# Performance work log

Hardware: AMD Instinct MI355X
Metric: run time of the kernel (lower is better)

## Reference

```python
import jax, jax.numpy as jnp
import numpy as np

EPS = 1e-6
K_MEM, C_MEM = 512, 2048
SEQ, BATCH = 256, 16
NUM_LAYERS, NUM_HEADS, HEAD_DIM = 12, 12, 64
KV_DIM = NUM_LAYERS * NUM_HEADS * HEAD_DIM * 2  # 18432
NOISE_STD = 0.01
PINV_STEPS = 3
BEN_COHEN_INIT = -5.0


def approx_pinv(A, steps=PINV_STEPS):
    # Ben-Cohen iterative pseudoinverse. A: (B, M, N) -> (B, N, M)
    alpha = jnp.minimum(jnp.exp(jnp.float32(BEN_COHEN_INIT)), jnp.float32(5e-4))  # clamp(max=5e-4)
    P = alpha * jnp.swapaxes(A, -2, -1)
    for _ in range(steps):
        P = 2.0 * P - (P @ A) @ P  # matches bmm(bmm(P, A), P)
    return P


def setup_inputs() -> dict:
    key = jax.random.key(0)
    ks = jax.random.split(key, 6)
    lim = np.sqrt(6.0 / (C_MEM + KV_DIM))  # xavier_uniform
    return {
        "z_sequence": jax.random.normal(ks[0], (SEQ, BATCH, C_MEM), jnp.float32),
        "z_query": jax.random.normal(ks[1], (BATCH, C_MEM), jnp.float32),
        "noise": jax.random.normal(ks[2], (SEQ, BATCH, C_MEM), jnp.float32),
        "memory_mean": jax.random.normal(ks[3], (K_MEM, C_MEM), jnp.float32) * 0.02,
        "memory_logvar": jnp.zeros((K_MEM,), jnp.float32),
        "w_logvar": jnp.zeros((1,), jnp.float32),
        "W_M_weight": jax.random.uniform(ks[4], (KV_DIM, C_MEM), jnp.float32, -lim, lim),
    }


def reference(z_sequence, z_query, noise, memory_mean, memory_logvar, w_logvar, W_M_weight):
    B = z_query.shape[0]
    # ---- write ----
    prior_var = jnp.exp(memory_logvar) + EPS                     # (K,)
    prior_mean_b = jnp.broadcast_to(memory_mean, (B, K_MEM, C_MEM))
    z_noise = z_sequence + noise * NOISE_STD                     # (S, B, C)
    z_t = jnp.swapaxes(z_noise, 0, 1)                            # (B, S, C)
    M_pinv = approx_pinv(prior_mean_b)                           # (B, C, K)
    w = z_t @ M_pinv                                             # (B, S, K)
    w_pinv = approx_pinv(w)                                      # (B, K, S)
    new_memory_mean = w_pinv @ z_t                               # (B, K, C)
    # KL divergence (post_var == prior_var here)
    t1 = C_MEM * jnp.sum(prior_var / prior_var)
    t2 = jnp.sum((new_memory_mean - prior_mean_b) ** 2 / prior_var[None, :, None], axis=(-2, -1))
    t3 = -jnp.float32(C_MEM * K_MEM)
    t4 = C_MEM * jnp.sum(jnp.log(prior_var) - jnp.log(prior_var))
    dkl_M = jnp.mean(t1 + t2 + t3 + t4)
    # ---- read (deterministic addressing) ----
    M_pinv2 = approx_pinv(new_memory_mean)                       # (B, C, K)
    w_mean = jnp.einsum('bc,bck->bk', z_query, M_pinv2)          # (B, K)
    z_retrieved = jnp.einsum('bk,bkc->bc', w_mean, new_memory_mean)  # (B, C)
    Z_r_kv = z_retrieved @ W_M_weight.T                          # (B, kv_dim)
    wl = jnp.broadcast_to(w_logvar, w_mean.shape)
    dkl_w = 0.5 * jnp.sum(jnp.exp(wl) + w_mean ** 2 - 1.0 - wl)
    return z_retrieved, Z_r_kv, dkl_M, dkl_w
```

## Files before the change

### kernel.cpp

```cpp
#include <hip/hip_runtime.h>

#define ALPHA 5.0e-4f

typedef short s16x8 __attribute__((ext_vector_type(8)));
typedef unsigned short u16x8 __attribute__((ext_vector_type(8)));
typedef float f32x4 __attribute__((ext_vector_type(4)));

__device__ __forceinline__ unsigned short f2bf(float f) {
    unsigned int u = __builtin_bit_cast(unsigned int, f);
    u += 0x7fffu + ((u >> 16) & 1u);
    return (unsigned short)(u >> 16);
}
__device__ __forceinline__ float bf2f(unsigned short h) {
    return __builtin_bit_cast(float, (unsigned int)h << 16);
}
__device__ __forceinline__ f32x4 mfma16(s16x8 a, s16x8 b, f32x4 c) {
    return __builtin_amdgcn_mfma_f32_16x16x32_bf16(a, b, c, 0, 0, 0);
}

template<int ROWS>
__device__ __forceinline__ void stage_kcontig(const float* __restrict__ src, int ld,
                                              unsigned short* __restrict__ lds, int tid)
{
#pragma unroll
    for (int it = 0; it < ROWS * 8 / 256; ++it) {
        const int g = tid + it * 256;
        const int row = g >> 3, s = g & 7;
        const float* p = src + (long long)row * ld + s * 8;
        const float4 x0 = *(const float4*)p;
        const float4 x1 = *(const float4*)(p + 4);
        u16x8 h;
        h[0] = f2bf(x0.x); h[1] = f2bf(x0.y); h[2] = f2bf(x0.z); h[3] = f2bf(x0.w);
        h[4] = f2bf(x1.x); h[5] = f2bf(x1.y); h[6] = f2bf(x1.z); h[7] = f2bf(x1.w);
        *(u16x8*)(lds + row * 64 + ((s ^ (row & 7)) << 3)) = h;
    }
}

template<int ROWS>
__device__ __forceinline__ void stage_kstrided(const float* __restrict__ src, int ld,
                                               unsigned short* __restrict__ lds, int tid)
{
    constexpr int KPT = ROWS * 64 / 256;
    const int m = tid % ROWS, kb = (tid / ROWS) * KPT;
#pragma unroll
    for (int j8 = 0; j8 < KPT / 8; ++j8) {
        u16x8 h;
#pragma unroll
        for (int j = 0; j < 8; ++j)
            h[j] = f2bf(src[(long long)(kb + j8 * 8 + j) * ld + m]);
        const int s = (kb >> 3) + j8;
        *(u16x8*)(lds + m * 64 + ((s ^ (m & 7)) << 3)) = h;
    }
}

template<int ROWS>
__device__ __forceinline__ void stage_kcontig_b(const unsigned short* __restrict__ src, int ld,
                                                unsigned short* __restrict__ lds, int tid)
{
#pragma unroll
    for (int it = 0; it < ROWS * 8 / 256; ++it) {
        const int g = tid + it * 256;
        const int row = g >> 3, s = g & 7;
        const u16x8 h = *(const u16x8*)(src + (long long)row * ld + s * 8);
        *(u16x8*)(lds + row * 64 + ((s ^ (row & 7)) << 3)) = h;
    }
}

template<int ROWS>
__device__ __forceinline__ void stage_kstrided_b(const unsigned short* __restrict__ src, int ld,
                                                 unsigned short* __restrict__ lds, int tid)
{
    constexpr int KPT = ROWS * 64 / 256;
    const int m = tid % ROWS, kb = (tid / ROWS) * KPT;
#pragma unroll
    for (int j8 = 0; j8 < KPT / 8; ++j8) {
        u16x8 h;
#pragma unroll
        for (int j = 0; j < 8; ++j)
            h[j] = src[(long long)(kb + j8 * 8 + j) * ld + m];
        const int s = (kb >> 3) + j8;
        *(u16x8*)(lds + m * 64 + ((s ^ (m & 7)) << 3)) = h;
    }
}

template<int BM, int BN, bool TA, bool TB, bool ABF, bool BBF, bool OBF,
         bool OT, bool CINT, bool ATOM = false>
__device__ __forceinline__
void gemm_dev(int bx, int by, int bz,
              const void* __restrict__ Av, int lda, long long sA,
              const void* __restrict__ Bv, int ldb, long long sB,
              void* __restrict__ Dv, int ldd, long long sD,
              const float* __restrict__ Cin, long long sC,
              float alpha, float beta, int Kd)
{
    constexpr int TWM = BM / 2, TWN = BN / 2;
    constexpr int FM = TWM / 16, FN = TWN / 16;
    __shared__ unsigned short As[BM * 64];
    __shared__ unsigned short Bs[BN * 64];

    const int tid = threadIdx.x;
    const int lane = tid & 63, w = tid >> 6;
    const int wm = w >> 1, wn = w & 1;
    const int lrow = lane & 15, lk = lane >> 4;
    const int m0 = by * BM, n0 = bx * BN;

    f32x4 acc[FM][FN];
#pragma unroll
    for (int i = 0; i < FM; ++i)
#pragma unroll
        for (int j = 0; j < FN; ++j) acc[i][j] = (f32x4){0.f, 0.f, 0.f, 0.f};

    for (int k0 = 0; k0 < Kd; k0 += 64) {
        if (ABF) {
            const unsigned short* Ab = (const unsigned short*)Av + (long long)bz * sA;
            if (!TA) stage_kcontig_b<BM>(Ab + (long long)m0 * lda + k0, lda, As, tid);
            else     stage_kstrided_b<BM>(Ab + (long long)k0 * lda + m0, lda, As, tid);
        } else {
            const float* Ab = (const float*)Av + (long long)bz * sA;
            if (!TA) stage_kcontig<BM>(Ab + (long long)m0 * lda + k0, lda, As, tid);
            else     stage_kstrided<BM>(Ab + (long long)k0 * lda + m0, lda, As, tid);
        }
        if (BBF) {
            const unsigned short* Bb = (const unsigned short*)Bv + (long long)bz * sB;
            if (TB)  stage_kcontig_b<BN>(Bb + (long long)n0 * ldb + k0, ldb, Bs, tid);
            else     stage_kstrided_b<BN>(Bb + (long long)k0 * ldb + n0, ldb, Bs, tid);
        } else {
            const float* Bb = (const float*)Bv + (long long)bz * sB;
            if (TB)  stage_kcontig<BN>(Bb + (long long)n0 * ldb + k0, ldb, Bs, tid);
            else     stage_kstrided<BN>(Bb + (long long)k0 * ldb + n0, ldb, Bs, tid);
        }
        __syncthreads();
#pragma unroll
        for (int kk = 0; kk < 2; ++kk) {
            s16x8 ah[FM], bh[FN];
#pragma unroll
            for (int i = 0; i < FM; ++i) {
                const int row = wm * TWM + i * 16 + lrow;
                const int s = kk * 4 + lk;
                ah[i] = *(const s16x8*)(As + row * 64 + ((s ^ (row & 7)) << 3));
            }
#pragma unroll
            for (int j = 0; j < FN; ++j) {
                const int col = wn * TWN + j * 16 + lrow;
                const int s = kk * 4 + lk;
                bh[j] = *(const s16x8*)(Bs + col * 64 + ((s ^ (col & 7)) << 3));
            }
#pragma unroll
            for (int i = 0; i < FM; ++i)
#pragma unroll
                for (int j = 0; j < FN; ++j)
                    acc[i][j] = mfma16(ah[i], bh[j], acc[i][j]);
        }
        __syncthreads();
    }

#pragma unroll
    for (int i = 0; i < FM; ++i)
#pragma unroll
        for (int j = 0; j < FN; ++j) {
            const int col = n0 + wn * TWN + j * 16 + lrow;
#pragma unroll
            for (int r = 0; r < 4; ++r) {
                const int row = m0 + wm * TWM + i * 16 + lk * 4 + r;
                float v = alpha * acc[i][j][r];
                if (Cin) {
                    const float cv = CINT ? Cin[(long long)col * sC + row]
                                          : Cin[(long long)row * ldd + col];
                    v = fmaf(beta, cv, v);
                }
                if (ATOM) {
                    atomicAdd((float*)Dv + (long long)row * ldd + col, v);
                } else if (OT) {
                    ((unsigned short*)Dv)[(long long)(row >> 8) * sD +
                                          (long long)col * ldd + (row & 255)] = f2bf(v);
                } else if (OBF) {
                    ((unsigned short*)Dv + (long long)bz * sD)[(long long)row * ldd + col] = f2bf(v);
                } else {
                    ((float*)Dv + (long long)bz * sD)[(long long)row * ldd + col] = v;
                }
            }
        }
}

template<int BM, int BN, bool TA, bool TB, bool ABF, bool BBF, bool OBF,
         bool OT = false, bool CINT = false>
__global__ __launch_bounds__(256)
void gemm_mfma(const void* __restrict__ Av, int lda, long long sA,
               const void* __restrict__ Bv, int ldb, long long sB,
               void* __restrict__ Dv, int ldd, long long sD,
               const float* __restrict__ Cin, long long sC,
               float alpha, float beta, int Kd)
{
    gemm_dev<BM, BN, TA, TB, ABF, BBF, OBF, OT, CINT>(
        blockIdx.x, blockIdx.y, blockIdx.z,
        Av, lda, sA, Bv, ldb, sB, Dv, ldd, sD, Cin, sC, alpha, beta, Kd);
}

__global__ __launch_bounds__(256)
void fused_prep_kernel(const float* __restrict__ zs, const float* __restrict__ no,
                       const float* __restrict__ zq, const float* __restrict__ mm,
                       unsigned short* __restrict__ ztb, float* __restrict__ q,
                       float* __restrict__ G1)
{
    const int blk = blockIdx.x, t = threadIdx.x;
    if (blk < 4096) {
        const int bs = blk;
        const int b = bs >> 8, sI = bs & 255;
        const long long in = ((long long)sI * 16 + b) * 2048 + t * 8;
        const f32x4 z0 = __builtin_nontemporal_load((const f32x4*)(zs + in));
        const f32x4 z1 = __builtin_nontemporal_load((const f32x4*)(zs + in + 4));
        const f32x4 n0 = __builtin_nontemporal_load((const f32x4*)(no + in));
        const f32x4 n1 = __builtin_nontemporal_load((const f32x4*)(no + in + 4));
        float zf[8];
#pragma unroll
        for (int j = 0; j < 4; ++j) {
            zf[j]     = fmaf(0.01f, n0[j], z0[j]);
            zf[j + 4] = fmaf(0.01f, n1[j], z1[j]);
        }
        u16x8 o;
#pragma unroll
        for (int j = 0; j < 8; ++j) o[j] = f2bf(zf[j]);
        *(u16x8*)(ztb + ((long long)bs * 2048 + t * 8)) = o;
        const float4 q0 = *(const float4*)(zq + b * 2048 + t * 8);
        const float4 q1 = *(const float4*)(zq + b * 2048 + t * 8 + 4);
        float qa = zf[0] * q0.x + zf[1] * q0.y + zf[2] * q0.z + zf[3] * q0.w
                 + zf[4] * q1.x + zf[5] * q1.y + zf[6] * q1.z + zf[7] * q1.w;
        __shared__ float red[256];
        red[t] = qa; __syncthreads();
        for (int st = 128; st > 0; st >>= 1) { if (t < st) red[t] += red[t + st]; __syncthreads(); }
        if (t == 0) q[bs] = red[0];
    } else {
        const int g = blk - 4096;
        const int ky = g & 7;
        const int tile = g >> 3;
        gemm_dev<64, 64, false, true, false, false, false, false, false, true>(
            tile & 7, tile >> 3, 0,
            mm + ky * 256, 2048, 0, mm + ky * 256, 2048, 0,
            G1, 512, 0, nullptr, 0, 1.f, 0.f, 256);
    }
}

__global__ __launch_bounds__(256)
void wT_u_kernel(const unsigned short* __restrict__ ztb,
                 const unsigned short* __restrict__ P1b,
                 unsigned short* __restrict__ wTb,
                 const float* __restrict__ q, float* __restrict__ wmean)
{
    constexpr int BM = 128, BN = 64, TWM = 64, TWN = 32, FM = 4, FN = 2;
    __shared__ unsigned short As[BM * 64];
    __shared__ unsigned short Bs[BN * 64];
    const int lin = blockIdx.x;
    const int r = lin & 7, tt = lin >> 3;
    const int by = r + 8 * (tt & 3), bx = tt >> 2;
    const int tid = threadIdx.x;
    const int lane = tid & 63, w = tid >> 6;
    const int wm = w >> 1, wn = w & 1;
    const int lrow = lane & 15, lk = lane >> 4;
    const int m0 = by * BM, n0 = bx * BN;

    f32x4 acc[FM][FN];
#pragma unroll
    for (int i = 0; i < FM; ++i)
#pragma unroll
        for (int j = 0; j < FN; ++j) acc[i][j] = (f32x4){0.f, 0.f, 0.f, 0.f};

    for (int k0 = 0; k0 < 2048; k0 += 64) {
        stage_kcontig_b<BM>(ztb + (long long)m0 * 2048 + k0, 2048, As, tid);
        stage_kstrided_b<BN>(P1b + (long long)k0 * 512 + n0, 512, Bs, tid);
        __syncthreads();
#pragma unroll
        for (int kk = 0; kk < 2; ++kk) {
            s16x8 ah[FM], bh[FN];
#pragma unroll
            for (int i = 0; i < FM; ++i) {
                const int row = wm * TWM + i * 16 + lrow;
                const int s = kk * 4 + lk;
                ah[i] = *(const s16x8*)(As + row * 64 + ((s ^ (row & 7)) << 3));
            }
#pragma unroll
            for (int j = 0; j < FN; ++j) {
                const int col = wn * TWN + j * 16 + lrow;
                const int s = kk * 4 + lk;
                bh[j] = *(const s16x8*)(Bs + col * 64 + ((s ^ (col & 7)) << 3));
            }
#pragma unroll
            for (int i = 0; i < FM; ++i)
#pragma unroll
                for (int j = 0; j < FN; ++j)
                    acc[i][j] = mfma16(ah[i], bh[j], acc[i][j]);
        }
        __syncthreads();
    }

    float up[FN] = {0.f, 0.f};
#pragma unroll
    for (int i = 0; i < FM; ++i)
#pragma unroll
        for (int rr = 0; rr < 4; ++rr) {
            const int row = m0 + wm * TWM + i * 16 + lk * 4 + rr;
            const float qv = q[row];
#pragma unroll
            for (int j = 0; j < FN; ++j) {
                const int col = n0 + wn * TWN + j * 16 + lrow;
                const float v = acc[i][j][rr];
                wTb[(long long)(row >> 8) * 131072 + (long long)col * 256 + (row & 255)] = f2bf(v);
                up[j] = fmaf(v, qv, up[j]);
            }
        }
    const int b = m0 >> 8;
#pragma unroll
    for (int j = 0; j < FN; ++j) {
        float v = up[j];
        v += __shfl_xor(v, 16);
        v += __shfl_xor(v, 32);
        if (lk == 0) {
            const int col = n0 + wn * TWN + j * 16 + lrow;
            atomicAdd(&wmean[b * 512 + col], (64.0f * ALPHA * ALPHA) * v);
        }
    }
}

__global__ __launch_bounds__(256)
void tail1_kernel(const unsigned short* __restrict__ wTb,
                  const unsigned short* __restrict__ ztb,
                  const float* __restrict__ wmean, const float* __restrict__ wlv,
                  float* __restrict__ out)
{
    __shared__ __align__(16) float smemf[1024];
    const int blk = blockIdx.x, tid = threadIdx.x;
    if (blk < 256) {
        float* wms = smemf;
        float* ys  = smemf + 512;
        float* red2 = smemf + 768;
        const int r8 = blk & 7, t8 = blk >> 3;
        const int b = r8 + 8 * (t8 & 1), ct = t8 >> 1;
        wms[tid] = wmean[b * 512 + tid];
        wms[tid + 256] = wmean[b * 512 + 256 + tid];
        __syncthreads();
        {
            const unsigned short* wp = wTb + (long long)b * 131072 + tid;
            float yv = 0.f;
#pragma unroll 8
            for (int k = 0; k < 512; ++k)
                yv = fmaf(wms[k], bf2f(wp[(long long)k * 256]), yv);
            ys[tid] = yv;
        }
        __syncthreads();
        const int c = ct * 128 + (tid & 127), sh = tid >> 7;
        const unsigned short* zp = ztb + (long long)b * 524288 + c;
        float acc2 = 0.f;
        const int sbase = sh * 128;
#pragma unroll 8
        for (int s = 0; s < 128; ++s)
            acc2 = fmaf(ys[sbase + s], bf2f(zp[(long long)(sbase + s) * 2048]), acc2);
        red2[tid] = acc2; __syncthreads();
        if (sh == 0)
            out[(long long)b * 2048 + c] = (8.0f * ALPHA) * (red2[tid] + red2[tid + 128]);
    } else {
        float* red = smemf;
        float s = 0.f;
        for (int i = tid; i < 16 * 512; i += 256) { const float v = wmean[i]; s += v * v; }
        red[tid] = s; __syncthreads();
        for (int st = 128; st > 0; st >>= 1) { if (tid < st) red[tid] += red[tid + st]; __syncthreads(); }
        if (tid == 0) {
            const float l = wlv[0];
            out[327681] = 0.5f * (red[0] + 8192.0f * (expf(l) - 1.0f - l));
        }
    }
}

__global__ __launch_bounds__(256)
void tail2_kernel(const unsigned short* __restrict__ wTb,
                  const unsigned short* __restrict__ ztb,
                  const float* __restrict__ mm, const float* __restrict__ mlv,
                  const float* __restrict__ WM, float* __restrict__ out)
{
    __shared__ __align__(16) unsigned char smem[34304];
    const int g = blockIdx.x, tid = threadIdx.x;
    const int grp = g / 26, p = g % 26;
    if (p < 8) {
        constexpr int BM = 128, BN = 128, TWM = 64, TWN = 64, FM = 4, FN = 4;
        unsigned short* As = (unsigned short*)smem;
        unsigned short* Bs = As + BM * 64;
        float* ivars = (float*)(smem + 32768);
        float* red = (float*)(smem + 33280);
        const int bz = ((2 * grp + p) & 7) + 8 * (grp & 1);
        const int rest = grp >> 1;
        const int by = rest & 3, bx = rest >> 2;
        const int lane = tid & 63, w = tid >> 6;
        const int wm = w >> 1, wn = w & 1;
        const int lrow = lane & 15, lk = lane >> 4;
        const int m0 = by * BM, n0 = bx * BN;

        if (tid < 128) ivars[tid] = 1.0f / (expf(mlv[m0 + tid]) + 1e-6f);

        f32x4 acc[FM][FN];
#pragma unroll
        for (int i = 0; i < FM; ++i)
#pragma unroll
            for (int j = 0; j < FN; ++j) acc[i][j] = (f32x4){0.f, 0.f, 0.f, 0.f};

        for (int k0 = 0; k0 < 256; k0 += 64) {
            stage_kcontig_b<BM>(wTb + (long long)bz * 131072 + (long long)m0 * 256 + k0, 256, As, tid);
            stage_kstrided_b<BN>(ztb + (long long)bz * 524288 + (long long)k0 * 2048 + n0, 2048, Bs, tid);
            __syncthreads();
#pragma unroll
            for (int kk = 0; kk < 2; ++kk) {
                s16x8 ah[FM], bh[FN];
#pragma unroll
                for (int i = 0; i < FM; ++i) {
                    const int row = wm * TWM + i * 16 + lrow;
                    const int s = kk * 4 + lk;
                    ah[i] = *(const s16x8*)(As + row * 64 + ((s ^ (row & 7)) << 3));
                }
#pragma unroll
                for (int j = 0; j < FN; ++j) {
                    const int col = wn * TWN + j * 16 + lrow;
                    const int s = kk * 4 + lk;
                    bh[j] = *(const s16x8*)(Bs + col * 64 + ((s ^ (col & 7)) << 3));
                }
#pragma unroll
                for (int i = 0; i < FM; ++i)
#pragma unroll
                    for (int j = 0; j < FN; ++j)
                        acc[i][j] = mfma16(ah[i], bh[j], acc[i][j]);
            }
            __syncthreads();
        }

        const float A8 = 8.0f * ALPHA;
        float da = 0.f;
#pragma unroll
        for (int i = 0; i < FM; ++i)
#pragma unroll
            for (int j = 0; j < FN; ++j) {
                const int cl = wn * TWN + j * 16 + lrow;
#pragma unroll
                for (int rr = 0; rr < 4; ++rr) {
                    const int rl = wm * TWM + i * 16 + lk * 4 + rr;
                    const float v = A8 * acc[i][j][rr];
                    const float d = v - mm[(long long)(m0 + rl) * 2048 + (n0 + cl)];
                    da = fmaf(d * d, ivars[rl], da);
                }
            }
        red[tid] = da; __syncthreads();
        for (int st = 128; st > 0; st >>= 1) { if (tid < st) red[tid] += red[tid + st]; __syncthreads(); }
        if (tid == 0) atomicAdd(&out[327680], red[0] * (1.0f / 16.0f));
    } else {
        const int z = grp * 18 + (p - 8);
        const int bx = z % 288, ky = z / 288;
        const int lane = tid & 63, w = tid >> 6;
        const int d0 = bx * 64 + w * 16;
        const int kc0 = ky * 256;
        const int rr = lane & 15, kq = lane >> 4;
        const float* zr = out;
        s16x8 areg[8];
        const float* zb = zr + rr * 2048 + kc0 + kq * 8;
#pragma unroll
        for (int s = 0; s < 8; ++s) {
            const f32x4 a0 = *(const f32x4*)(zb + s * 32);
            const f32x4 a1 = *(const f32x4*)(zb + s * 32 + 4);
            u16x8 h;
#pragma unroll
            for (int j = 0; j < 4; ++j) { h[j] = f2bf(a0[j]); h[j + 4] = f2bf(a1[j]); }
            areg[s] = __builtin_bit_cast(s16x8, h);
        }
        f32x4 acc = {0.f, 0.f, 0.f, 0.f};
        const float* wb = WM + (long long)(d0 + rr) * 2048 + kc0 + kq * 8;
#pragma unroll
        for (int s = 0; s < 8; ++s) {
            const f32x4 b0 = __builtin_nontemporal_load((const f32x4*)(wb + s * 32));
            const f32x4 b1 = __builtin_nontemporal_load((const f32x4*)(wb + s * 32 + 4));
            u16x8 h;
#pragma unroll
            for (int j = 0; j < 4; ++j) { h[j] = f2bf(b0[j]); h[j + 4] = f2bf(b1[j]); }
            acc = mfma16(areg[s], __builtin_bit_cast(s16x8, h), acc);
        }
        float* oz = out + 32768;
#pragma unroll
        for (int r = 0; r < 4; ++r)
            atomicAdd(&oz[(long long)(kq * 4 + r) * 18432 + d0 + rr], acc[r]);
    }
}

extern "C" void kernel_launch(void* const* d_in, const int* in_sizes, int n_in,
                              void* d_out, int out_size, void* d_ws, size_t ws_size,
                              hipStream_t stream)
{
    (void)in_sizes; (void)n_in; (void)out_size; (void)ws_size;
    const float* z_seq   = (const float*)d_in[0];
    const float* z_query = (const float*)d_in[1];
    const float* noise   = (const float*)d_in[2];
    const float* mm      = (const float*)d_in[3];
    const float* mlv     = (const float*)d_in[4];
    const float* wlv     = (const float*)d_in[5];
    const float* WM      = (const float*)d_in[6];
    float* out = (float*)d_out;

    char* wsb = (char*)d_ws;
    unsigned short* ztb  = (unsigned short*)(wsb);
    unsigned short* wTb  = (unsigned short*)(wsb + (16LL << 20));
    float*          G1   = (float*)(wsb + (24LL << 20));
    float*          wmean = (float*)(wsb + (25LL << 20));
    unsigned short* P1b  = (unsigned short*)(wsb + (26LL << 20));
    float*          qvec = (float*)(wsb + (30LL << 20));

    hipMemsetAsync(G1, 0, (1u << 20) + 32768, stream);
    hipMemsetAsync(out + 32768, 0, (294912 + 1) * sizeof(float), stream);
    fused_prep_kernel<<<4608, 256, 0, stream>>>(z_seq, noise, z_query, mm,
                                                ztb, qvec, G1);
    gemm_mfma<64,64,true,false,false,false,true,false,true><<<dim3(8,32,1),256,0,stream>>>(
        mm,2048,0, G1,512,0, P1b,512,0, mm,2048,
        -28.0f*ALPHA*ALPHA, 8.0f*ALPHA, 512);
    wT_u_kernel<<<256,256,0,stream>>>(ztb, P1b, wTb, qvec, wmean);
    tail1_kernel<<<257,256,0,stream>>>(wTb, ztb, wmean, wlv, out);
    tail2_kernel<<<3328,256,0,stream>>>(wTb, ztb, mm, mlv, WM, out);
}
```

Before: 177.6 us.

## Replace atomic split-K Gram with partial buffers, fold memsets into P1 kernel

```diff
diff --git a/kernel.cpp b/kernel.cpp
--- a/kernel.cpp
+++ b/kernel.cpp
@@ -83,15 +83,12 @@
     }
 }
 
-template<int BM, int BN, bool TA, bool TB, bool ABF, bool BBF, bool OBF,
-         bool OT, bool CINT, bool ATOM = false>
+template<int BM, int BN, bool TA, bool TB>
 __device__ __forceinline__
-void gemm_dev(int bx, int by, int bz,
-              const void* __restrict__ Av, int lda, long long sA,
-              const void* __restrict__ Bv, int ldb, long long sB,
-              void* __restrict__ Dv, int ldd, long long sD,
-              const float* __restrict__ Cin, long long sC,
-              float alpha, float beta, int Kd)
+void gemm_dev_f32(int bx, int by,
+                  const float* __restrict__ A, int lda,
+                  const float* __restrict__ B, int ldb,
+                  float* __restrict__ D, int ldd, int Kd)
 {
     constexpr int TWM = BM / 2, TWN = BN / 2;
     constexpr int FM = TWM / 16, FN = TWN / 16;
@@ -111,24 +108,10 @@
         for (int j = 0; j < FN; ++j) acc[i][j] = (f32x4){0.f, 0.f, 0.f, 0.f};
 
     for (int k0 = 0; k0 < Kd; k0 += 64) {
-        if (ABF) {
-            const unsigned short* Ab = (const unsigned short*)Av + (long long)bz * sA;
-            if (!TA) stage_kcontig_b<BM>(Ab + (long long)m0 * lda + k0, lda, As, tid);
-            else     stage_kstrided_b<BM>(Ab + (long long)k0 * lda + m0, lda, As, tid);
-        } else {
-            const float* Ab = (const float*)Av + (long long)bz * sA;
-            if (!TA) stage_kcontig<BM>(Ab + (long long)m0 * lda + k0, lda, As, tid);
-            else     stage_kstrided<BM>(Ab + (long long)k0 * lda + m0, lda, As, tid);
-        }
-        if (BBF) {
-            const unsigned short* Bb = (const unsigned short*)Bv + (long long)bz * sB;
-            if (TB)  stage_kcontig_b<BN>(Bb + (long long)n0 * ldb + k0, ldb, Bs, tid);
-            else     stage_kstrided_b<BN>(Bb + (long long)k0 * ldb + n0, ldb, Bs, tid);
-        } else {
-            const float* Bb = (const float*)Bv + (long long)bz * sB;
-            if (TB)  stage_kcontig<BN>(Bb + (long long)n0 * ldb + k0, ldb, Bs, tid);
-            else     stage_kstrided<BN>(Bb + (long long)k0 * ldb + n0, ldb, Bs, tid);
-        }
+        if (!TA) stage_kcontig<BM>(A + (long long)m0 * lda + k0, lda, As, tid);
+        else     stage_kstrided<BM>(A + (long long)k0 * lda + m0, lda, As, tid);
+        if (TB)  stage_kcontig<BN>(B + (long long)n0 * ldb + k0, ldb, Bs, tid);
+        else     stage_kstrided<BN>(B + (long long)k0 * ldb + n0, ldb, Bs, tid);
         __syncthreads();
 #pragma unroll
         for (int kk = 0; kk < 2; ++kk) {
@@ -162,49 +145,28 @@
 #pragma unroll
             for (int r = 0; r < 4; ++r) {
                 const int row = m0 + wm * TWM + i * 16 + lk * 4 + r;
-                float v = alpha * acc[i][j][r];
-                if (Cin) {
-                    const float cv = CINT ? Cin[(long long)col * sC + row]
-                                          : Cin[(long long)row * ldd + col];
-                    v = fmaf(beta, cv, v);
-                }
-                if (ATOM) {
-                    atomicAdd((float*)Dv + (long long)row * ldd + col, v);
-                } else if (OT) {
-                    ((unsigned short*)Dv)[(long long)(row >> 8) * sD +
-                                          (long long)col * ldd + (row & 255)] = f2bf(v);
-                } else if (OBF) {
-                    ((unsigned short*)Dv + (long long)bz * sD)[(long long)row * ldd + col] = f2bf(v);
-                } else {
-                    ((float*)Dv + (long long)bz * sD)[(long long)row * ldd + col] = v;
-                }
-            }
-        }
-}
-
-template<int BM, int BN, bool TA, bool TB, bool ABF, bool BBF, bool OBF,
-         bool OT = false, bool CINT = false>
-__global__ __launch_bounds__(256)
-void gemm_mfma(const void* __restrict__ Av, int lda, long long sA,
-               const void* __restrict__ Bv, int ldb, long long sB,
-               void* __restrict__ Dv, int ldd, long long sD,
-               const float* __restrict__ Cin, long long sC,
-               float alpha, float beta, int Kd)
-{
-    gemm_dev<BM, BN, TA, TB, ABF, BBF, OBF, OT, CINT>(
-        blockIdx.x, blockIdx.y, blockIdx.z,
-        Av, lda, sA, Bv, ldb, sB, Dv, ldd, sD, Cin, sC, alpha, beta, Kd);
+                D[(long long)row * ldd + col] = acc[i][j][r];
+            }
+        }
 }
 
 __global__ __launch_bounds__(256)
 void fused_prep_kernel(const float* __restrict__ zs, const float* __restrict__ no,
                        const float* __restrict__ zq, const float* __restrict__ mm,
                        unsigned short* __restrict__ ztb, float* __restrict__ q,
-                       float* __restrict__ G1)
+                       float* __restrict__ Gp)
 {
     const int blk = blockIdx.x, t = threadIdx.x;
-    if (blk < 4096) {
-        const int bs = blk;
+    if (blk % 9 == 8) {
+        const int g = blk / 9;
+        const int ky = g & 7;
+        const int tile = g >> 3;
+        gemm_dev_f32<64, 64, false, true>(
+            tile & 7, tile >> 3,
+            mm + ky * 256, 2048, mm + ky * 256, 2048,
+            Gp + (long long)ky * 262144, 512, 256);
+    } else {
+        const int bs = blk - blk / 9;
         const int b = bs >> 8, sI = bs & 255;
         const long long in = ((long long)sI * 16 + b) * 2048 + t * 8;
         const f32x4 z0 = __builtin_nontemporal_load((const f32x4*)(zs + in));
@@ -229,14 +191,99 @@
         red[t] = qa; __syncthreads();
         for (int st = 128; st > 0; st >>= 1) { if (t < st) red[t] += red[t + st]; __syncthreads(); }
         if (t == 0) q[bs] = red[0];
+    }
+}
+
+__global__ __launch_bounds__(256)
+void p1_zero_kernel(const float* __restrict__ mm, const float* __restrict__ Gp,
+                    unsigned short* __restrict__ P1b,
+                    float* __restrict__ wmean, float* __restrict__ out)
+{
+    const int blk = blockIdx.x, tid = threadIdx.x;
+    if (blk < 256) {
+        constexpr int BM = 64, BN = 64, TWM = 32, TWN = 32, FM = 2, FN = 2;
+        __shared__ unsigned short As[BM * 64];
+        __shared__ unsigned short Bs[BN * 64];
+        const int bx = blk & 7, by = blk >> 3;
+        const int lane = tid & 63, w = tid >> 6;
+        const int wm = w >> 1, wn = w & 1;
+        const int lrow = lane & 15, lk = lane >> 4;
+        const int m0 = by * BM, n0 = bx * BN;
+
+        f32x4 acc[FM][FN];
+#pragma unroll
+        for (int i = 0; i < FM; ++i)
+#pragma unroll
+            for (int j = 0; j < FN; ++j) acc[i][j] = (f32x4){0.f, 0.f, 0.f, 0.f};
+
+        for (int k0 = 0; k0 < 512; k0 += 64) {
+            stage_kstrided<BM>(mm + (long long)k0 * 2048 + m0, 2048, As, tid);
+            {
+                const int m = tid & 63, kb = (tid >> 6) * 16;
+#pragma unroll
+                for (int j8 = 0; j8 < 2; ++j8) {
+                    u16x8 h;
+#pragma unroll
+                    for (int j = 0; j < 8; ++j) {
+                        const long long off = (long long)(k0 + kb + j8 * 8 + j) * 512 + n0 + m;
+                        float s = 0.f;
+#pragma unroll
+                        for (int p = 0; p < 8; ++p) s += Gp[(long long)p * 262144 + off];
+                        h[j] = f2bf(s);
+                    }
+                    const int sl = (kb >> 3) + j8;
+                    *(u16x8*)(Bs + m * 64 + ((sl ^ (m & 7)) << 3)) = h;
+                }
+            }
+            __syncthreads();
+#pragma unroll
+            for (int kk = 0; kk < 2; ++kk) {
+                s16x8 ah[FM], bh[FN];
+#pragma unroll
+                for (int i = 0; i < FM; ++i) {
+                    const int row = wm * TWM + i * 16 + lrow;
+                    const int s = kk * 4 + lk;
+                    ah[i] = *(const s16x8*)(As + row * 64 + ((s ^ (row & 7)) << 3));
+                }
+#pragma unroll
+                for (int j = 0; j < FN; ++j) {
+                    const int col = wn * TWN + j * 16 + lrow;
+                    const int s = kk * 4 + lk;
+                    bh[j] = *(const s16x8*)(Bs + col * 64 + ((s ^ (col & 7)) << 3));
+                }
+#pragma unroll
+                for (int i = 0; i < FM; ++i)
+#pragma unroll
+                    for (int j = 0; j < FN; ++j)
+                        acc[i][j] = mfma16(ah[i], bh[j], acc[i][j]);
+            }
+            __syncthreads();
+        }
+
+        const float al = -28.0f * ALPHA * ALPHA, be = 8.0f * ALPHA;
+#pragma unroll
+        for (int i = 0; i < FM; ++i)
+#pragma unroll
+            for (int j = 0; j < FN; ++j) {
+                const int col = n0 + wn * TWN + j * 16 + lrow;
+#pragma unroll
+                for (int r = 0; r < 4; ++r) {
+                    const int row = m0 + wm * TWM + i * 16 + lk * 4 + r;
+                    const float v = fmaf(be, mm[(long long)col * 2048 + row], al * acc[i][j][r]);
+                    P1b[(long long)row * 512 + col] = f2bf(v);
+                }
+            }
     } else {
-        const int g = blk - 4096;
-        const int ky = g & 7;
-        const int tile = g >> 3;
-        gemm_dev<64, 64, false, true, false, false, false, false, false, true>(
-            tile & 7, tile >> 3, 0,
-            mm + ky * 256, 2048, 0, mm + ky * 256, 2048, 0,
-            G1, 512, 0, nullptr, 0, 1.f, 0.f, 256);
+        const int zb = blk - 256;
+        float4* oz = (float4*)(out + 32768);
+        const int base = (zb * 256 + tid) * 32;
+#pragma unroll
+        for (int i = 0; i < 32; ++i) oz[base + i] = (float4){0.f, 0.f, 0.f, 0.f};
+        if (zb == 0) {
+            float4* wm4 = (float4*)wmean;
+            for (int i = tid; i < 2048; i += 256) wm4[i] = (float4){0.f, 0.f, 0.f, 0.f};
+            if (tid == 0) out[327680] = 0.f;
+        }
     }
 }
 
@@ -246,12 +293,12 @@
                  unsigned short* __restrict__ wTb,
                  const float* __restrict__ q, float* __restrict__ wmean)
 {
-    constexpr int BM = 128, BN = 64, TWM = 64, TWN = 32, FM = 4, FN = 2;
+    constexpr int BM = 64, BN = 64, TWM = 32, TWN = 32, FM = 2, FN = 2;
     __shared__ unsigned short As[BM * 64];
     __shared__ unsigned short Bs[BN * 64];
     const int lin = blockIdx.x;
-    const int r = lin & 7, tt = lin >> 3;
-    const int by = r + 8 * (tt & 3), bx = tt >> 2;
+    const int r = lin & 7, t = lin >> 3;
+    const int by = r + 8 * (t & 7), bx = t >> 3;
     const int tid = threadIdx.x;
     const int lane = tid & 63, w = tid >> 6;
     const int wm = w >> 1, wn = w & 1;
@@ -500,19 +547,15 @@
     char* wsb = (char*)d_ws;
     unsigned short* ztb  = (unsigned short*)(wsb);
     unsigned short* wTb  = (unsigned short*)(wsb + (16LL << 20));
-    float*          G1   = (float*)(wsb + (24LL << 20));
-    float*          wmean = (float*)(wsb + (25LL << 20));
-    unsigned short* P1b  = (unsigned short*)(wsb + (26LL << 20));
-    float*          qvec = (float*)(wsb + (30LL << 20));
-
-    hipMemsetAsync(G1, 0, (1u << 20) + 32768, stream);
-    hipMemsetAsync(out + 32768, 0, (294912 + 1) * sizeof(float), stream);
+    float*          Gp   = (float*)(wsb + (24LL << 20));
+    unsigned short* P1b  = (unsigned short*)(wsb + (32LL << 20));
+    float*          qvec = (float*)(wsb + (36LL << 20));
+    float*          wmean = (float*)(wsb + (37LL << 20));
+
     fused_prep_kernel<<<4608, 256, 0, stream>>>(z_seq, noise, z_query, mm,
-                                                ztb, qvec, G1);
-    gemm_mfma<64,64,true,false,false,false,true,false,true><<<dim3(8,32,1),256,0,stream>>>(
-        mm,2048,0, G1,512,0, P1b,512,0, mm,2048,
-        -28.0f*ALPHA*ALPHA, 8.0f*ALPHA, 512);
-    wT_u_kernel<<<256,256,0,stream>>>(ztb, P1b, wTb, qvec, wmean);
-    tail1_kernel<<<257,256,0,stream>>>(wTb, ztb, wmean, wlv, out);
-    tail2_kernel<<<3328,256,0,stream>>>(wTb, ztb, mm, mlv, WM, out);
-}
+                                                ztb, qvec, Gp);
+    p1_zero_kernel<<<265, 256, 0, stream>>>(mm, Gp, P1b, wmean, out);
+    wT_u_kernel<<<512, 256, 0, stream>>>(ztb, P1b, wTb, qvec, wmean);
+    tail1_kernel<<<257, 256, 0, stream>>>(wTb, ztb, wmean, wlv, out);
+    tail2_kernel<<<3328, 256, 0, stream>>>(wTb, ztb, mm, mlv, WM, out);
+}
```

Measured after the change: 255.0 us. +43.6%, slower.
